# Kernel optimization log

Hardware: AMD Instinct MI355X
Metric: run time of the kernel (lower is better)

## Reference

```python
import jax, jax.numpy as jnp
import numpy as np
import math

HIDDEN = 1024
N_HEADS = 16
HEAD_DIM = HIDDEN // N_HEADS

def _safe(x, clamp_val):
    x = jnp.nan_to_num(x, nan=0.0, posinf=0.0, neginf=0.0)
    return jnp.clip(x, -clamp_val, clamp_val)

def _stable_linear(x, W, b):
    # StableLinear: clamp(50) -> linear -> clamp(50)
    x = _safe(x, 50.0)
    out = x @ W.T + b
    return _safe(out, 50.0)

def setup_inputs() -> dict:
    key = jax.random.key(0)
    ks = jax.random.split(key, 12)
    bsz, q_len, kv_len = 4, 1024, 2048
    q = jax.random.normal(ks[0], (bsz, q_len, HIDDEN), dtype=jnp.float32)
    kv = jax.random.normal(ks[1], (bsz, kv_len, HIDDEN), dtype=jnp.float32)
    key_padding_mask = jax.random.bernoulli(ks[2], 0.1, (bsz, kv_len))
    bound = 1.0 / math.sqrt(HIDDEN)
    def mk_w(k):
        return jax.random.uniform(k, (HIDDEN, HIDDEN), jnp.float32, -bound, bound)
    def mk_b(k):
        return jax.random.uniform(k, (HIDDEN,), jnp.float32, -bound, bound)
    return {
        'q': q, 'kv': kv, 'key_padding_mask': key_padding_mask,
        'Wq': mk_w(ks[3]), 'bq': mk_b(ks[4]),
        'Wk': mk_w(ks[5]), 'bk': mk_b(ks[6]),
        'Wv': mk_w(ks[7]), 'bv': mk_b(ks[8]),
        'Wo': mk_w(ks[9]), 'bo': mk_b(ks[10]),
    }

def reference(q, kv, key_padding_mask, Wq, bq, Wk, bk, Wv, bv, Wo, bo):
    bsz, q_len, _ = q.shape
    kv_len = kv.shape[1]
    # outer _safe(50) then StableLinear's own _safe(50) (idempotent)
    qh = _stable_linear(_safe(q, 50.0), Wq, bq)
    kh = _stable_linear(_safe(kv, 50.0), Wk, bk)
    vh = _stable_linear(_safe(kv, 50.0), Wv, bv)
    # [b, h, s, d]
    qh = qh.reshape(bsz, q_len, N_HEADS, HEAD_DIM).transpose(0, 2, 1, 3)
    kh = kh.reshape(bsz, kv_len, N_HEADS, HEAD_DIM).transpose(0, 2, 1, 3)
    vh = vh.reshape(bsz, kv_len, N_HEADS, HEAD_DIM).transpose(0, 2, 1, 3)
    scores = jnp.einsum('bhqd,bhkd->bhqk', qh.astype(jnp.float32), kh.astype(jnp.float32))
    scores = scores / math.sqrt(HEAD_DIM)
    scores = jnp.clip(scores, -80.0, 80.0)
    scores = jnp.where(key_padding_mask[:, None, None, :], -10000.0, scores)
    attn = jax.nn.softmax(scores, axis=-1)  # dropout is identity in eval mode
    out = jnp.einsum('bhqk,bhkd->bhqd', attn, vh.astype(jnp.float32))
    out = out.transpose(0, 2, 1, 3).reshape(bsz, q_len, HIDDEN)
    out = _stable_linear(_safe(out, 50.0), Wo, bo)
    return _safe(out, 50.0)
```

## Files before the change

kernel.cpp:

```cpp
#include <hip/hip_runtime.h>
#include <hip/hip_bf16.h>
#include <stdint.h>
#include <math.h>

#define HIDDEN 1024
#define NHEADS 16
#define HDIM   64
#define BSZ    4
#define QLEN   1024
#define KVLEN  2048

typedef __bf16 bf16_t;
typedef __bf16 bf16x8 __attribute__((ext_vector_type(8)));
typedef __bf16 bf16x4 __attribute__((ext_vector_type(4)));
typedef float  f32x4  __attribute__((ext_vector_type(4)));

#define C_SCALE 0.18033688f
#define C_FMADD (-43.2808512f)

#define GLOAD16(g, l) \
    __builtin_amdgcn_global_load_lds((const __attribute__((address_space(1))) void*)(g), \
                                     (__attribute__((address_space(3))) void*)(l), 16, 0, 0)

__device__ __forceinline__ float clamp50(float v) {
    return fminf(fmaxf(v, -50.f), 50.f);
}

#define NQ4  ((BSZ * QLEN  * HIDDEN) / 4)
#define NKV4 ((BSZ * KVLEN * HIDDEN) / 4)
#define NW4  ((HIDDEN * HIDDEN) / 4)
#define NCVT ((NQ4 + NKV4 + 4 * NW4) / 256)

__global__ void cvt_all_kernel(const float* __restrict__ q, const float* __restrict__ kv,
                               const float* __restrict__ W0, const float* __restrict__ W1,
                               const float* __restrict__ W2, const float* __restrict__ W3,
                               bf16_t* __restrict__ q_bf, bf16_t* __restrict__ kv_bf,
                               bf16_t* __restrict__ w_bf,
                               const void* __restrict__ msk, float* __restrict__ maskadd) {
    if (blockIdx.x >= NCVT) {
        __shared__ int s_float, s_multi;
        const int t = threadIdx.x;
        if (t == 0) { s_float = 0; s_multi = 0; }
        __syncthreads();
        const uint32_t* w = (const uint32_t*)msk;
        int cf = 0, cm = 0;
        for (int i = t; i < 2048; i += 256) {
            uint32_t v = w[i];
            if (v == 0x3F800000u) cf++;
            else if (v & 0xFFFFFF00u) cm++;
        }
        if (cf) atomicAdd(&s_float, cf);
        if (cm) atomicAdd(&s_multi, cm);
        __syncthreads();
        const int mode = (s_float > 0) ? 2 : ((s_multi > 0) ? 0 : 1);
        const int base = (blockIdx.x - NCVT) * 2048;
        for (int i = base + t; i < base + 2048; i += 256) {
            bool m;
            if (mode == 2)      m = ((const float*)msk)[i] != 0.0f;
            else if (mode == 1) m = ((const int*)msk)[i] != 0;
            else                m = ((const unsigned char*)msk)[i] != 0;
            maskadd[i] = m ? (-100000.0f + C_FMADD) : C_FMADD;
        }
        return;
    }
    const int i = blockIdx.x * blockDim.x + threadIdx.x;
    const float4* src;
    bf16x4* dst;
    if (i < NQ4) {
        src = (const float4*)q + i;            dst = (bf16x4*)q_bf + i;
    } else if (i < NQ4 + NKV4) {
        const int j = i - NQ4;
        src = (const float4*)kv + j;           dst = (bf16x4*)kv_bf + j;
    } else {
        const int j = i - (NQ4 + NKV4);
        const int ws = j >> 18, off = j & (NW4 - 1);
        const float* W = (ws == 0) ? W0 : (ws == 1) ? W1 : (ws == 2) ? W2 : W3;
        src = (const float4*)W + off;          dst = (bf16x4*)w_bf + (size_t)ws * NW4 + off;
    }
    const float4 v = *src;
    bf16x4 o;
    o[0] = (bf16_t)clamp50(v.x); o[1] = (bf16_t)clamp50(v.y);
    o[2] = (bf16_t)clamp50(v.z); o[3] = (bf16_t)clamp50(v.w);
    *dst = o;
}

template <int NT>
__device__ __forceinline__ void gemm_core(const char* __restrict__ Ab, const char* __restrict__ Bb,
                                          bf16_t* Als, bf16_t* Bls,
                                          f32x4 (&acc)[4][NT / 32],
                                          int wave, int lane, int wm, int wn)
{
    constexpr int NF = NT / 32;
    const int srcsw = ((lane & 7) ^ (lane >> 3)) << 4;
    const int rowl = lane >> 3;

    for (int kt = 0; kt < HIDDEN / 64; ++kt) {
#pragma unroll
        for (int i = 0; i < 4; ++i) {
            const int row = i * 32 + wave * 8 + rowl;
            GLOAD16(Ab + (size_t)row * (HIDDEN * 2) + kt * 128 + srcsw,
                    (char*)Als + i * 4096 + wave * 1024);
        }
#pragma unroll
        for (int i = 0; i < NF; ++i) {
            const int row = i * 32 + wave * 8 + rowl;
            GLOAD16(Bb + (size_t)row * (HIDDEN * 2) + kt * 128 + srcsw,
                    (char*)Bls + i * 4096 + wave * 1024);
        }
        __syncthreads();
#pragma unroll
        for (int kc = 0; kc < 2; ++kc) {
            const int kbyte = kc * 64 + ((lane >> 4) << 4);
            bf16x8 af[4], bfr[NF];
#pragma unroll
            for (int f2 = 0; f2 < 4; ++f2) {
                const int arow = wm * 64 + f2 * 16 + (lane & 15);
                af[f2] = *(const bf16x8*)((const char*)Als + arow * 128 + (kbyte ^ ((arow & 7) << 4)));
            }
#pragma unroll
            for (int f2 = 0; f2 < NF; ++f2) {
                const int brow = wn * (NT / 2) + f2 * 16 + (lane & 15);
                bfr[f2] = *(const bf16x8*)((const char*)Bls + brow * 128 + (kbyte ^ ((brow & 7) << 4)));
            }
#pragma unroll
            for (int mf = 0; mf < 4; ++mf)
#pragma unroll
                for (int nf = 0; nf < NF; ++nf)
                    acc[mf][nf] = __builtin_amdgcn_mfma_f32_16x16x32_bf16(af[mf], bfr[nf], acc[mf][nf], 0, 0, 0);
        }
        __syncthreads();
    }
}

template <int NF>
__device__ __forceinline__ void epi_head(f32x4 (&acc)[4][NF], const float* bias,
                                         bf16_t* out, int m0, int n0, int slog,
                                         int wm, int wn, int lane)
{
#pragma unroll
    for (int mf = 0; mf < 4; ++mf) {
#pragma unroll
        for (int nf = 0; nf < NF; ++nf) {
            const int gn = n0 + wn * (NF * 16) + nf * 16 + (lane & 15);
            const float bv = bias[gn];
#pragma unroll
            for (int r = 0; r < 4; ++r) {
                const int gm = m0 + wm * 64 + mf * 16 + ((lane >> 4) << 2) + r;
                const float v = clamp50(acc[mf][nf][r] + bv);
                const int b = gm >> slog;
                const int s = gm & ((1 << slog) - 1);
                const int h = gn >> 6, d = gn & 63;
                out[((((size_t)(b * NHEADS + h)) << slog) + s) * HDIM + d] = (bf16_t)v;
            }
        }
    }
}

__global__ __launch_bounds__(256)
void gemm_proj_all(const bf16_t* __restrict__ q_bf, const bf16_t* __restrict__ kv_bf,
                   const bf16_t* __restrict__ w_bf,
                   const float* __restrict__ bq, const float* __restrict__ bk,
                   const float* __restrict__ bv,
                   bf16_t* __restrict__ qh, bf16_t* __restrict__ kh,
                   bf16_t* __restrict__ vt)
{
    __shared__ __align__(16) bf16_t Smem[2 * 128 * 64];
    bf16_t* Als = Smem;
    bf16_t* Bls = Smem + 128 * 64;

    const int bid = blockIdx.x;
    const int lid = (bid & 7) * 160 + (bid >> 3);

    int seg, j;
    if (lid < 256)      { seg = 0; j = lid; }
    else if (lid < 768) { seg = 1; j = lid - 256; }
    else                { seg = 2; j = lid - 768; }
    const int m0 = (j >> 3) * 128;
    const int n0 = (j & 7) * 128;
    const bf16_t* A    = (seg == 0) ? q_bf : kv_bf;
    const bf16_t* B    = w_bf + (size_t)seg * (HIDDEN * HIDDEN);
    const float*  bias = (seg == 0) ? bq : (seg == 1) ? bk : bv;

    const int t = threadIdx.x;
    const int wave = t >> 6, lane = t & 63;
    const int wm = wave >> 1, wn = wave & 1;

    f32x4 acc[4][4] = {};
    gemm_core<128>((const char*)A + (size_t)m0 * (HIDDEN * 2),
                   (const char*)B + (size_t)n0 * (HIDDEN * 2),
                   Als, Bls, acc, wave, lane, wm, wn);

    if (seg == 0) {
        epi_head<4>(acc, bias, qh, m0, n0, 10, wm, wn, lane);
        return;
    }
    if (seg == 1) {
        epi_head<4>(acc, bias, kh, m0, n0, 11, wm, wn, lane);
        return;
    }

    bf16_t* Cls = Smem;
    const int dl = t >> 1;
    const int sh = (t & 1) << 5;
    const int gn = n0 + dl;
    const int h = gn >> 6, d = gn & 63;
    const int bb = m0 >> 11;
    bf16_t* dst = vt + ((size_t)((bb * NHEADS + h) * HDIM + d)) * KVLEN
                + (m0 & (KVLEN - 1)) + sh;
#pragma unroll
    for (int ph = 0; ph < 2; ++ph) {
        if (wm == ph) {
#pragma unroll
            for (int mf = 0; mf < 4; ++mf) {
#pragma unroll
                for (int nf = 0; nf < 4; ++nf) {
                    const int dcol = wn * 64 + nf * 16 + (lane & 15);
                    const float bv2 = bias[n0 + dcol];
#pragma unroll
                    for (int r = 0; r < 4; ++r) {
                        const int srow = mf * 16 + ((lane >> 4) << 2) + r;
                        Cls[srow * 130 + dcol] = (bf16_t)clamp50(acc[mf][nf][r] + bv2);
                    }
                }
            }
        }
        __syncthreads();
#pragma unroll
        for (int j0 = 0; j0 < 32; j0 += 8) {
            bf16x8 v;
#pragma unroll
            for (int jj = 0; jj < 8; ++jj) v[jj] = Cls[(sh + j0 + jj) * 130 + dl];
            *(bf16x8*)(dst + ph * 64 + j0) = v;
        }
        __syncthreads();
    }
}

template <int NT>
__global__ __launch_bounds__(256)
void gemm_out_kernel(const bf16_t* __restrict__ A, const bf16_t* __restrict__ B,
                     const float* __restrict__ bias, float* __restrict__ out)
{
    constexpr int NF = NT / 32;
    __shared__ __align__(16) bf16_t Smem[(128 + NT) * 64];
    bf16_t* Als = Smem;
    bf16_t* Bls = Smem + 128 * 64;

    const int m0 = blockIdx.y * 128;
    const int n0 = blockIdx.x * NT;
    const int t = threadIdx.x;
    const int wave = t >> 6, lane = t & 63;
    const int wm = wave >> 1, wn = wave & 1;

    f32x4 acc[4][NF] = {};
    gemm_core<NT>((const char*)A + (size_t)m0 * (HIDDEN * 2),
                  (const char*)B + (size_t)n0 * (HIDDEN * 2),
                  Als, Bls, acc, wave, lane, wm, wn);

#pragma unroll
    for (int mf = 0; mf < 4; ++mf) {
#pragma unroll
        for (int nf = 0; nf < NF; ++nf) {
            const int gn = n0 + wn * (NF * 16) + nf * 16 + (lane & 15);
            const float bv = bias[gn];
#pragma unroll
            for (int r = 0; r < 4; ++r) {
                const int gm = m0 + wm * 64 + mf * 16 + ((lane >> 4) << 2) + r;
                out[(size_t)gm * HIDDEN + gn] = clamp50(acc[mf][nf][r] + bv);
            }
        }
    }
}

__global__ __launch_bounds__(512)
void attn_fwd_kernel(const bf16_t* __restrict__ Qh, const bf16_t* __restrict__ Kh,
                     const bf16_t* __restrict__ Vt, const float* __restrict__ maskadd,
                     bf16_t* __restrict__ aout)
{
    __shared__ __align__(16) bf16_t Kls[2][64 * 64];
    __shared__ __align__(16) bf16_t Vls[2][64 * 64];
    __shared__ __align__(16) float Cbuf[4][32 * 64];
    __shared__ float Lbuf[4][2][16];

    const int f = blockIdx.x;
    const int o = (f & 7) * 64 + (f >> 3);
    const int qt = o & 7;
    const int bh = o >> 3;
    const int b = bh >> 4, h = bh & 15;
    const int t = threadIdx.x, wave = t >> 6, lane = t & 63;
    const int wq = wave & 3;
    const int wg = wave >> 2;
    const int g = lane >> 4, ql = lane & 15;

    const int qbase = qt * 128 + wq * 32;
    bf16x8 qf[2][2];
#pragma unroll
    for (int qq = 0; qq < 2; ++qq) {
        const bf16_t* qp = Qh + ((size_t)bh * QLEN + qbase + qq * 16 + ql) * HDIM + (g << 3);
        qf[qq][0] = *(const bf16x8*)qp;
        qf[qq][1] = *(const bf16x8*)(qp + 32);
    }

    f32x4 oacc[2][4] = {};
    float lsum[2] = {0.f, 0.f};

    const int srcsw = ((lane & 7) ^ (lane >> 3)) << 4;
    const int R = wave * 8 + (lane >> 3);
    const int kap = 32 * (R >> 5) + 8 * ((R >> 2) & 3) + 4 * ((R >> 4) & 1) + (R & 3);

    const char* Kb = (const char*)(Kh + (size_t)bh * KVLEN * HDIM);
    const char* Vb = (const char*)(Vt + (size_t)bh * HDIM * KVLEN);
    const float* mrow = maskadd + b * KVLEN + wg * 32 + g * 8;
    const int kb0 = g << 4;
    const int vcol = wg * 64 + kb0;

    GLOAD16(Kb + (size_t)kap * 128 + srcsw, (char*)&Kls[0][0] + wave * 1024);
    GLOAD16(Vb + (size_t)R * (KVLEN * 2) + srcsw, (char*)&Vls[0][0] + wave * 1024);
    f32x4 madd_c[2], madd_n[2];
    madd_c[0] = *(const f32x4*)(mrow);
    madd_c[1] = *(const f32x4*)(mrow + 4);
    __syncthreads();

    for (int kt = 0; kt < KVLEN / 64; ++kt) {
        const int cur = kt & 1;
        if (kt < KVLEN / 64 - 1) {
            const size_t ko = (size_t)(kt + 1) * 8192;
            GLOAD16(Kb + ko + (size_t)kap * 128 + srcsw,
                    (char*)&Kls[cur ^ 1][0] + wave * 1024);
            GLOAD16(Vb + (size_t)R * (KVLEN * 2) + (size_t)(kt + 1) * 128 + srcsw,
                    (char*)&Vls[cur ^ 1][0] + wave * 1024);
            madd_n[0] = *(const f32x4*)(mrow + (kt + 1) * 64);
            madd_n[1] = *(const f32x4*)(mrow + (kt + 1) * 64 + 4);
        }
        const char* Kc = (const char*)&Kls[cur][0];
        const char* Vc = (const char*)&Vls[cur][0];

        f32x4 sacc[2][2] = {};
        __builtin_amdgcn_s_setprio(1);
#pragma unroll
        for (int kb = 0; kb < 2; ++kb) {
            const int key = wg * 32 + kb * 16 + ql;
            const int rowoff = key * 128;
            const int sw = (key & 7) << 4;
            const bf16x8 kf0 = *(const bf16x8*)(Kc + rowoff + ((kb0)      ^ sw));
            const bf16x8 kf1 = *(const bf16x8*)(Kc + rowoff + ((kb0 + 64) ^ sw));
#pragma unroll
            for (int qq = 0; qq < 2; ++qq) {
                sacc[qq][kb] = __builtin_amdgcn_mfma_f32_16x16x32_bf16(kf0, qf[qq][0], sacc[qq][kb], 0, 0, 0);
                sacc[qq][kb] = __builtin_amdgcn_mfma_f32_16x16x32_bf16(kf1, qf[qq][1], sacc[qq][kb], 0, 0, 0);
            }
        }
        __builtin_amdgcn_s_setprio(0);

        bf16x8 pa[2];
#pragma unroll
        for (int qq = 0; qq < 2; ++qq) {
            float pv[2][4];
            float ls = 0.f;
#pragma unroll
            for (int kb = 0; kb < 2; ++kb) {
#pragma unroll
                for (int r = 0; r < 4; ++r) {
                    pv[kb][r] = __builtin_amdgcn_exp2f(
                        __builtin_fmaf(sacc[qq][kb][r], C_SCALE, madd_c[kb][r]));
                    ls += pv[kb][r];
                }
            }
            lsum[qq] += ls;
#pragma unroll
            for (int r = 0; r < 4; ++r) {
                pa[qq][r]     = (bf16_t)pv[0][r];
                pa[qq][4 + r] = (bf16_t)pv[1][r];
            }
        }

        __builtin_amdgcn_s_setprio(1);
#pragma unroll
        for (int db = 0; db < 4; ++db) {
            const int vrow = db * 16 + ql;
            const int vsw = (vrow & 7) << 4;
            const bf16x8 vf = *(const bf16x8*)(Vc + vrow * 128 + (vcol ^ vsw));
#pragma unroll
            for (int qq = 0; qq < 2; ++qq)
                oacc[qq][db] = __builtin_amdgcn_mfma_f32_16x16x32_bf16(pa[qq], vf, oacc[qq][db], 0, 0, 0);
        }
        __builtin_amdgcn_s_setprio(0);

        __syncthreads();
#pragma unroll
        for (int kb = 0; kb < 2; ++kb) madd_c[kb] = madd_n[kb];
    }

#pragma unroll
    for (int qq = 0; qq < 2; ++qq) {
        float l = lsum[qq];
        l += __shfl_xor(l, 16);
        l += __shfl_xor(l, 32);
        lsum[qq] = l;
    }
    const int rbase = g << 2;
    if (wg == 1) {
#pragma unroll
        for (int qq = 0; qq < 2; ++qq) {
#pragma unroll
            for (int db = 0; db < 4; ++db)
#pragma unroll
                for (int r = 0; r < 4; ++r)
                    Cbuf[wq][(qq * 16 + rbase + r) * 64 + db * 16 + ql] = oacc[qq][db][r];
            if (lane < 16) Lbuf[wq][qq][lane] = lsum[qq];
        }
    }
    __syncthreads();
    if (wg == 0) {
#pragma unroll
        for (int qq = 0; qq < 2; ++qq) {
            const float Lq = lsum[qq] + Lbuf[wq][qq][ql];
#pragma unroll
            for (int r = 0; r < 4; ++r) {
                const float Lr = __shfl(Lq, rbase + r);
                const float inv = 1.0f / Lr;
                const int qrow = qbase + qq * 16 + rbase + r;
                bf16_t* orow = aout + ((size_t)(b * QLEN + qrow)) * HIDDEN + h * HDIM;
#pragma unroll
                for (int db = 0; db < 4; ++db) {
                    const float add = Cbuf[wq][(qq * 16 + rbase + r) * 64 + db * 16 + ql];
                    orow[db * 16 + ql] = (bf16_t)((oacc[qq][db][r] + add) * inv);
                }
            }
        }
    }
}

extern "C" void kernel_launch(void* const* d_in, const int* in_sizes, int n_in,
                              void* d_out, int out_size, void* d_ws, size_t ws_size,
                              hipStream_t stream) {
    (void)in_sizes; (void)n_in; (void)out_size; (void)ws_size;
    const float* q   = (const float*)d_in[0];
    const float* kv  = (const float*)d_in[1];
    const void*  msk = d_in[2];
    const float* Wq  = (const float*)d_in[3];
    const float* bq  = (const float*)d_in[4];
    const float* Wk  = (const float*)d_in[5];
    const float* bk  = (const float*)d_in[6];
    const float* Wv  = (const float*)d_in[7];
    const float* bv  = (const float*)d_in[8];
    const float* Wo  = (const float*)d_in[9];
    const float* bo  = (const float*)d_in[10];

    char* ws = (char*)d_ws;
    const size_t MB = 1024 * 1024;
    float*  maskadd = (float*)ws;
    bf16_t* w_bf  = (bf16_t*)(ws + 32 * 1024);
    bf16_t* q_bf  = (bf16_t*)(ws + 32 * 1024 + 8  * MB);
    bf16_t* kv_bf = (bf16_t*)(ws + 32 * 1024 + 16 * MB);
    bf16_t* qh    = (bf16_t*)(ws + 32 * 1024 + 32 * MB);
    bf16_t* kh    = (bf16_t*)(ws + 32 * 1024 + 40 * MB);
    bf16_t* vt    = (bf16_t*)(ws + 32 * 1024 + 56 * MB);
    bf16_t* aout  = q_bf;

    bf16_t* wo_bf = w_bf + (size_t)3 * HIDDEN * HIDDEN;

    cvt_all_kernel<<<dim3(NCVT + 4), 256, 0, stream>>>(
        q, kv, Wq, Wk, Wv, Wo, q_bf, kv_bf, w_bf, msk, maskadd);

    gemm_proj_all<<<dim3(1280), 256, 0, stream>>>(
        q_bf, kv_bf, w_bf, bq, bk, bv, qh, kh, vt);

    attn_fwd_kernel<<<dim3(512), 512, 0, stream>>>(qh, kh, vt, maskadd, aout);

    gemm_out_kernel<64><<<dim3(16, 32), 256, 0, stream>>>(aout, wo_bf, bo, (float*)d_out);
}
```

Measured before the change: 153.9 us.

## Double-buffer LDS tiles in projection and output GEMMs, remap output block order

The shared GEMM core now prefetches the next K tile into a second LDS buffer with global_load_lds while MFMAs run on the current tile. The aim is to overlap global-to-LDS transfer with compute and drop one barrier per K step. LDS per block doubles, to 64 KB in the projection GEMM, which can lower occupancy. The output GEMM also moves to a 1D grid with an interleaved block-to-tile mapping, meant to improve cache locality across the XCDs.

After: 146.6 us. 1.05x faster.

```diff
diff --git a/kernel.cpp b/kernel.cpp
--- a/kernel.cpp
+++ b/kernel.cpp
@@ -85,29 +85,46 @@
 }
 
 template <int NT>
-__device__ __forceinline__ void gemm_core(const char* __restrict__ Ab, const char* __restrict__ Bb,
-                                          bf16_t* Als, bf16_t* Bls,
-                                          f32x4 (&acc)[4][NT / 32],
-                                          int wave, int lane, int wm, int wn)
+__device__ __forceinline__ void stage_tile(const char* __restrict__ Ab,
+                                           const char* __restrict__ Bb,
+                                           char* base, int kt, int wave, int rowl, int srcsw)
 {
     constexpr int NF = NT / 32;
+#pragma unroll
+    for (int i = 0; i < 4; ++i) {
+        const int row = i * 32 + wave * 8 + rowl;
+        GLOAD16(Ab + (size_t)row * (HIDDEN * 2) + kt * 128 + srcsw,
+                base + i * 4096 + wave * 1024);
+    }
+#pragma unroll
+    for (int i = 0; i < NF; ++i) {
+        const int row = i * 32 + wave * 8 + rowl;
+        GLOAD16(Bb + (size_t)row * (HIDDEN * 2) + kt * 128 + srcsw,
+                base + 16384 + i * 4096 + wave * 1024);
+    }
+}
+
+template <int NT>
+__device__ __forceinline__ void gemm_core_db(const char* __restrict__ Ab,
+                                             const char* __restrict__ Bb,
+                                             char* Ls,
+                                             f32x4 (&acc)[4][NT / 32],
+                                             int wave, int lane, int wm, int wn)
+{
+    constexpr int NF = NT / 32;
+    constexpr int BUF = (128 + NT) * 128;
     const int srcsw = ((lane & 7) ^ (lane >> 3)) << 4;
     const int rowl = lane >> 3;
 
+    stage_tile<NT>(Ab, Bb, Ls, 0, wave, rowl, srcsw);
+    __syncthreads();
+
     for (int kt = 0; kt < HIDDEN / 64; ++kt) {
-#pragma unroll
-        for (int i = 0; i < 4; ++i) {
-            const int row = i * 32 + wave * 8 + rowl;
-            GLOAD16(Ab + (size_t)row * (HIDDEN * 2) + kt * 128 + srcsw,
-                    (char*)Als + i * 4096 + wave * 1024);
-        }
-#pragma unroll
-        for (int i = 0; i < NF; ++i) {
-            const int row = i * 32 + wave * 8 + rowl;
-            GLOAD16(Bb + (size_t)row * (HIDDEN * 2) + kt * 128 + srcsw,
-                    (char*)Bls + i * 4096 + wave * 1024);
-        }
-        __syncthreads();
+        const int cur = kt & 1;
+        if (kt < HIDDEN / 64 - 1)
+            stage_tile<NT>(Ab, Bb, Ls + (cur ^ 1) * BUF, kt + 1, wave, rowl, srcsw);
+        const char* Abase = Ls + cur * BUF;
+        const char* Bbase = Abase + 16384;
 #pragma unroll
         for (int kc = 0; kc < 2; ++kc) {
             const int kbyte = kc * 64 + ((lane >> 4) << 4);
@@ -115,12 +132,12 @@
 #pragma unroll
             for (int f2 = 0; f2 < 4; ++f2) {
                 const int arow = wm * 64 + f2 * 16 + (lane & 15);
-                af[f2] = *(const bf16x8*)((const char*)Als + arow * 128 + (kbyte ^ ((arow & 7) << 4)));
+                af[f2] = *(const bf16x8*)(Abase + arow * 128 + (kbyte ^ ((arow & 7) << 4)));
             }
 #pragma unroll
             for (int f2 = 0; f2 < NF; ++f2) {
                 const int brow = wn * (NT / 2) + f2 * 16 + (lane & 15);
-                bfr[f2] = *(const bf16x8*)((const char*)Bls + brow * 128 + (kbyte ^ ((brow & 7) << 4)));
+                bfr[f2] = *(const bf16x8*)(Bbase + brow * 128 + (kbyte ^ ((brow & 7) << 4)));
             }
 #pragma unroll
             for (int mf = 0; mf < 4; ++mf)
@@ -164,9 +181,7 @@
                    bf16_t* __restrict__ qh, bf16_t* __restrict__ kh,
                    bf16_t* __restrict__ vt)
 {
-    __shared__ __align__(16) bf16_t Smem[2 * 128 * 64];
-    bf16_t* Als = Smem;
-    bf16_t* Bls = Smem + 128 * 64;
+    __shared__ __align__(16) bf16_t Smem[2 * 256 * 64];
 
     const int bid = blockIdx.x;
     const int lid = (bid & 7) * 160 + (bid >> 3);
@@ -186,9 +201,9 @@
     const int wm = wave >> 1, wn = wave & 1;
 
     f32x4 acc[4][4] = {};
-    gemm_core<128>((const char*)A + (size_t)m0 * (HIDDEN * 2),
-                   (const char*)B + (size_t)n0 * (HIDDEN * 2),
-                   Als, Bls, acc, wave, lane, wm, wn);
+    gemm_core_db<128>((const char*)A + (size_t)m0 * (HIDDEN * 2),
+                      (const char*)B + (size_t)n0 * (HIDDEN * 2),
+                      (char*)Smem, acc, wave, lane, wm, wn);
 
     if (seg == 0) {
         epi_head<4>(acc, bias, qh, m0, n0, 10, wm, wn, lane);
@@ -207,6 +222,7 @@
     const int bb = m0 >> 11;
     bf16_t* dst = vt + ((size_t)((bb * NHEADS + h) * HDIM + d)) * KVLEN
                 + (m0 & (KVLEN - 1)) + sh;
+    __syncthreads();
 #pragma unroll
     for (int ph = 0; ph < 2; ++ph) {
         if (wm == ph) {
@@ -236,26 +252,26 @@
     }
 }
 
-template <int NT>
 __global__ __launch_bounds__(256)
 void gemm_out_kernel(const bf16_t* __restrict__ A, const bf16_t* __restrict__ B,
                      const float* __restrict__ bias, float* __restrict__ out)
 {
+    constexpr int NT = 64;
     constexpr int NF = NT / 32;
-    __shared__ __align__(16) bf16_t Smem[(128 + NT) * 64];
-    bf16_t* Als = Smem;
-    bf16_t* Bls = Smem + 128 * 64;
-
-    const int m0 = blockIdx.y * 128;
-    const int n0 = blockIdx.x * NT;
+    __shared__ __align__(16) bf16_t Smem[2 * (128 + NT) * 64];
+
+    const int bid = blockIdx.x;
+    const int lid = (bid & 7) * 64 + (bid >> 3);
+    const int m0 = (lid >> 4) * 128;
+    const int n0 = (lid & 15) * NT;
     const int t = threadIdx.x;
     const int wave = t >> 6, lane = t & 63;
     const int wm = wave >> 1, wn = wave & 1;
 
     f32x4 acc[4][NF] = {};
-    gemm_core<NT>((const char*)A + (size_t)m0 * (HIDDEN * 2),
-                  (const char*)B + (size_t)n0 * (HIDDEN * 2),
-                  Als, Bls, acc, wave, lane, wm, wn);
+    gemm_core_db<NT>((const char*)A + (size_t)m0 * (HIDDEN * 2),
+                     (const char*)B + (size_t)n0 * (HIDDEN * 2),
+                     (char*)Smem, acc, wave, lane, wm, wn);
 
 #pragma unroll
     for (int mf = 0; mf < 4; ++mf) {
@@ -468,5 +484,5 @@
 
     attn_fwd_kernel<<<dim3(512), 512, 0, stream>>>(qh, kh, vt, maskadd, aout);
 
-    gemm_out_kernel<64><<<dim3(16, 32), 256, 0, stream>>>(aout, wo_bf, bo, (float*)d_out);
-}
+    gemm_out_kernel<<<dim3(512), 256, 0, stream>>>(aout, wo_bf, bo, (float*)d_out);
+}
```
